# Kernel optimization log

Measured on AMD Instinct MI355X. Metric: run time of the kernel, lower is better.

## Reference

```python
import jax, jax.numpy as jnp
import numpy as np

# Network dims (see init_kwargs)
T, B, N_IN, N_HID, N_OUT = 1000, 256, 128, 512, 128
DT = 0.05
SPIKE_R = 20.0
K_M = 0.2
R_HID = 0.1 + 1.0 / N_HID   # Rs[k] = R + 1/sizes[k]
THRESH = 0.0
V_RESET = 0.0
SIGMA_V = 50.0
I0 = 700.0
ASC_AMP = np.array([-1.0, 1.0], np.float32)
ASC_R = np.array([1.0, -1.0], np.float32)
ASC_K = np.array([3.0, 30.0], np.float32)


def setup_inputs() -> dict:
    key = jax.random.key(0)
    ks = jax.random.split(key, 5)
    s_in = 1.0 / np.sqrt(N_IN)
    s_hid = 1.0 / np.sqrt(N_HID)
    return {
        "inputs": jax.random.normal(ks[0], (T, B, N_IN), jnp.float32),
        "W_in": jax.random.uniform(ks[1], (N_HID, N_IN), jnp.float32, -s_in, s_in),
        "b_in": jnp.zeros((N_HID,), jnp.float32),
        "W_rec": jax.random.uniform(ks[2], (N_HID, N_HID), jnp.float32, -s_hid, s_hid),
        "W_out": jax.random.uniform(ks[3], (N_OUT, N_HID), jnp.float32, -s_hid, s_hid),
        "b_out": jnp.zeros((N_OUT,), jnp.float32),
    }


def reference(inputs, W_in, b_in, W_rec, W_out, b_out):
    """BNN3L forward: per timestep, hidden GLIFR layer receives the average of
    the input projection (current-step placeholder spikes) and the recurrent
    projection of its own spikes delayed by 1 step; the output placeholder
    stores the linear readout of the current hidden spikes.
    Returns stacked output-layer spikes_all: [T, B, N_OUT]."""
    asc_amp = jnp.asarray(ASC_AMP)[:, None, None]
    asc_r = jnp.asarray(ASC_R)[:, None, None]
    asc_k = jnp.asarray(ASC_K)[:, None, None]

    def step(carry, x_t):
        v, asc, s = carry  # v,s: [B,H]; asc: [2,B,H]
        # average of the two incoming connections (n_in = 2)
        y = (x_t @ W_in.T + b_in + s @ W_rec.T) * 0.5
        # after-spike currents (Euler)
        asc = asc * (1.0 - DT * asc_k) + DT * asc_r * asc_amp * s
        i_tot = y + asc.sum(0) + I0
        # membrane voltage with continuous soft reset driven by firing rate s
        v = v * (1.0 - DT * K_M) * (1.0 - DT * s) + DT * s * V_RESET \
            + DT * K_M * R_HID * i_tot
        # rate-coded "spike" output
        s = SPIKE_R * jax.nn.sigmoid((v - THRESH) / SIGMA_V)
        # output placeholder: linear readout of current hidden spikes (delay 1 forced)
        out = s @ W_out.T + b_out
        return (v, asc, s), out

    v0 = jnp.zeros((B, N_HID), jnp.float32)
    asc0 = jnp.zeros((2, B, N_HID), jnp.float32)
    s0 = jnp.zeros((B, N_HID), jnp.float32)
    _, outs = jax.lax.scan(step, (v0, asc0, s0), inputs)
    return outs
```

## Files before the change

kernel.cpp:

```cpp
#include <hip/hip_runtime.h>

#define T_STEPS 1000
#define BATCH   256
#define NIN     128
#define NHID    512
#define NOUT    128
#define ROWS    16
#define HGRP    4
#define HCOLS   128
#define NCLU    16
#define CLUSZ   4

typedef _Float16 half8   __attribute__((ext_vector_type(8)));
typedef float    floatx4 __attribute__((ext_vector_type(4)));

__device__ __forceinline__ half8 f8_to_h8(const float* __restrict__ p) {
  floatx4 lo = *(const floatx4*)p;
  floatx4 hi = *(const floatx4*)(p + 4);
  half8 r;
#pragma unroll
  for (int i = 0; i < 4; ++i) { r[i] = (_Float16)lo[i]; r[i + 4] = (_Float16)hi[i]; }
  return r;
}

#define EX_OFF 1024

__global__ void init_ws_kernel(char* __restrict__ ws) {
  size_t idx = (size_t)blockIdx.x * blockDim.x + threadIdx.x;
  ((int4*)(ws + EX_OFF))[idx] = make_int4(0, 0, 0, 0);
  if (blockIdx.x == 0 && threadIdx.x < NCLU)
    *(unsigned int*)(ws + threadIdx.x * 64) = 0u;
}

#define PBUF 131072

__global__ __launch_bounds__(256, 1) void bnn_cluster_kernel(
    const float* __restrict__ X,
    const float* __restrict__ Win,
    const float* __restrict__ bin,
    const float* __restrict__ Wrec,
    const float* __restrict__ Wout,
    const float* __restrict__ bout,
    float* __restrict__ out,
    char* __restrict__ ws)
{
  __shared__ __attribute__((aligned(16))) char smem[135168];
  const int tid = threadIdx.x;
  const int l   = tid & 63;
  const int w   = tid >> 6;
  const int lr  = l & 15;
  const int lq  = l >> 4;
  const int bi  = blockIdx.x & 15;
  const int hj  = blockIdx.x >> 4;
  const int m0  = bi * ROWS;
  const int cw  = hj * HCOLS + w * 32;
  const int oj  = hj * 32;
  const int tw  = w & 1;
  const int kh  = w >> 1;

  unsigned int* cnt = (unsigned int*)(ws + (size_t)bi * 64);
  _Float16* ex = (_Float16*)(ws + EX_OFF);

#pragma unroll
  for (int tt = 0; tt < 2; ++tt)
#pragma unroll
    for (int kk = 0; kk < 16; ++kk) {
      half8 v = f8_to_h8(Wrec + (size_t)(cw + tt*16 + lr) * NHID + kk*32 + lq*8);
      *(half8*)(smem + (((w*2 + tt)*16 + kk) * 64 + l) * 16) = v;
    }

  half8 win[2][4];
#pragma unroll
  for (int tt = 0; tt < 2; ++tt)
#pragma unroll
    for (int kk = 0; kk < 4; ++kk)
      win[tt][kk] = f8_to_h8(Win + (size_t)(cw + tt*16 + lr) * NIN + kk*32 + lq*8);

  half8 wo[8];
#pragma unroll
  for (int i = 0; i < 8; ++i)
    wo[i] = f8_to_h8(Wout + (size_t)(oj + tw*16 + lr) * NHID + (kh*8 + i)*32 + lq*8);

  const float binv0 = bin[cw + lr];
  const float binv1 = bin[cw + 16 + lr];
  const float bo    = bout[oj + tw*16 + lr];

  float v[8], a0[8], a1[8], sp[8];
#pragma unroll
  for (int i = 0; i < 8; ++i) { v[i] = 0.f; a0[i] = 0.f; a1[i] = 0.f; sp[i] = 0.f; }

  floatx4 rop;
  rop[0] = rop[1] = rop[2] = rop[3] = 0.f;

  const float C_VI = (float)(0.05 * 0.2 * (0.1 + 1.0 / 512.0));

#pragma unroll 1
  for (int t = 0; t <= T_STEPS; ++t) {
    floatx4 xlo[4], xhi[4];
    if (t < T_STEPS) {
      const float* xt = X + ((size_t)t * BATCH + m0 + lr) * NIN + lq * 8;
#pragma unroll
      for (int kk = 0; kk < 4; ++kk) {
        xlo[kk] = *(const floatx4*)(xt + kk * 32);
        xhi[kk] = *(const floatx4*)(xt + kk * 32 + 4);
      }
    }

    __syncthreads();
    if (tid == 0) {
      __threadfence();
      atomicAdd(cnt, 1u);
      const unsigned int tgt = (unsigned int)CLUSZ * (unsigned int)(t + 1);
      while (__hip_atomic_load(cnt, __ATOMIC_RELAXED, __HIP_MEMORY_SCOPE_AGENT) < tgt)
        __builtin_amdgcn_s_sleep(2);
    }
    __syncthreads();
    __threadfence();

    const _Float16* sprev = ex + (size_t)(t & 1) * 131072 + (size_t)bi * 8192;
    half8 sfr[16];
#pragma unroll
    for (int kk = 0; kk < 16; ++kk)
      sfr[kk] = *(const half8*)(sprev + kk * 512 + l * 8);

    if (t >= 2 && w < 2) {
      floatx4 pp = *(const floatx4*)(smem + PBUF + ((t - 1) & 1) * 2048 + tw * 1024 + l * 16);
      float* op = out + ((size_t)(t - 2) * BATCH + m0 + lq * 4) * NOUT + oj + tw * 16 + lr;
#pragma unroll
      for (int r = 0; r < 4; ++r) op[(size_t)r * NOUT] = rop[r] + pp[r] + bo;
    }

    if (t >= 1) {
      floatx4 rp;
      rp[0] = rp[1] = rp[2] = rp[3] = 0.f;
#pragma unroll
      for (int i = 0; i < 8; ++i)
        rp = __builtin_amdgcn_mfma_f32_16x16x32_f16(sfr[kh*8 + i], wo[i], rp, 0, 0, 0);
      if (w >= 2) *(floatx4*)(smem + PBUF + (t & 1) * 2048 + tw * 1024 + l * 16) = rp;
      else        rop = rp;
    }

    if (t < T_STEPS) {
      floatx4 acc[2];
      acc[0][0] = acc[0][1] = acc[0][2] = acc[0][3] = binv0;
      acc[1][0] = acc[1][1] = acc[1][2] = acc[1][3] = binv1;
#pragma unroll
      for (int kk = 0; kk < 16; ++kk) {
#pragma unroll
        for (int tt = 0; tt < 2; ++tt) {
          half8 wb = *(const half8*)(smem + (((w*2 + tt)*16 + kk) * 64 + l) * 16);
          acc[tt] = __builtin_amdgcn_mfma_f32_16x16x32_f16(sfr[kk], wb, acc[tt], 0, 0, 0);
        }
      }
#pragma unroll
      for (int kk = 0; kk < 4; ++kk) {
        half8 xa;
#pragma unroll
        for (int i = 0; i < 4; ++i) {
          xa[i]     = (_Float16)xlo[kk][i];
          xa[i + 4] = (_Float16)xhi[kk][i];
        }
#pragma unroll
        for (int tt = 0; tt < 2; ++tt)
          xa, acc[tt] = __builtin_amdgcn_mfma_f32_16x16x32_f16(xa, win[tt][kk], acc[tt], 0, 0, 0);
      }

      _Float16* scur = ex + (size_t)((t + 1) & 1) * 131072 + (size_t)bi * 8192;
#pragma unroll
      for (int tt = 0; tt < 2; ++tt)
#pragma unroll
        for (int r = 0; r < 4; ++r) {
          const int i = tt*4 + r;
          const float y  = 0.5f * acc[tt][r];
          a0[i] = a0[i] * 0.85f - 0.05f * sp[i];
          a1[i] = a1[i] * -0.5f - 0.05f * sp[i];
          const float it = y + a0[i] + a1[i] + 700.0f;
          v[i] = v[i] * 0.99f * (1.0f - 0.05f * sp[i]) + C_VI * it;
          const float s = 20.0f / (1.0f + __expf(-0.02f * v[i]));
          sp[i] = s;
          const int koff  = tt*16 + lr;
          const int lane2 = (lq*4 + r) + 16*(koff >> 3);
          scur[(hj*4 + w)*512 + lane2*8 + (koff & 7)] = (_Float16)s;
        }
    }
  }

  __syncthreads();
  if (w < 2) {
    floatx4 pp = *(const floatx4*)(smem + PBUF + (T_STEPS & 1) * 2048 + tw * 1024 + l * 16);
    float* op = out + ((size_t)(T_STEPS - 1) * BATCH + m0 + lq * 4) * NOUT + oj + tw * 16 + lr;
#pragma unroll
    for (int r = 0; r < 4; ++r) op[(size_t)r * NOUT] = rop[r] + pp[r] + bo;
  }
}

extern "C" void kernel_launch(void* const* d_in, const int* in_sizes, int n_in,
                              void* d_out, int out_size, void* d_ws, size_t ws_size,
                              hipStream_t stream) {
  const float* X    = (const float*)d_in[0];
  const float* Win  = (const float*)d_in[1];
  const float* bin  = (const float*)d_in[2];
  const float* Wrec = (const float*)d_in[3];
  const float* Wout = (const float*)d_in[4];
  const float* bout = (const float*)d_in[5];
  float* out = (float*)d_out;
  char* ws = (char*)d_ws;

  hipLaunchKernelGGL(init_ws_kernel, dim3(128), dim3(256), 0, stream, ws);
  hipLaunchKernelGGL(bnn_cluster_kernel, dim3(NCLU * HGRP), dim3(256), 0, stream,
                     X, Win, bin, Wrec, Wout, bout, out, ws);
}
```

Baseline: 9.236 ms.

## Replace cluster atomic counter barrier with per-wave flag handshakes

Swaps the per-cluster atomicAdd counter barrier (one thread spinning with sleep, surrounded by __syncthreads and threadfences) for per-wave ready flags. Each wave stages its spike fragment in LDS, publishes it to global memory with relaxed agent-scope stores, then sets its own flag. Consumer waves poll the 16 flags with a ballot, so no thread spins alone and the full fences are gone. This cuts cross-block synchronisation latency on every timestep, but it depends on relaxed ordering plus vmcnt waits being enough for visibility, and it adds a block-wide barrier at the end of each step.

```diff
diff --git a/kernel.cpp b/kernel.cpp
--- a/kernel.cpp
+++ b/kernel.cpp
@@ -6,13 +6,11 @@
 #define NHID    512
 #define NOUT    128
 #define ROWS    16
-#define HGRP    4
-#define HCOLS   128
 #define NCLU    16
-#define CLUSZ   4
 
 typedef _Float16 half8   __attribute__((ext_vector_type(8)));
 typedef float    floatx4 __attribute__((ext_vector_type(4)));
+typedef unsigned long long u64;
 
 __device__ __forceinline__ half8 f8_to_h8(const float* __restrict__ p) {
   floatx4 lo = *(const floatx4*)p;
@@ -23,18 +21,17 @@
   return r;
 }
 
-#define EX_OFF 1024
+#define DATA_OFF 32768
 
 __global__ void init_ws_kernel(char* __restrict__ ws) {
   size_t idx = (size_t)blockIdx.x * blockDim.x + threadIdx.x;
-  ((int4*)(ws + EX_OFF))[idx] = make_int4(0, 0, 0, 0);
-  if (blockIdx.x == 0 && threadIdx.x < NCLU)
-    *(unsigned int*)(ws + threadIdx.x * 64) = 0u;
-}
-
-#define PBUF 131072
-
-__global__ __launch_bounds__(256, 1) void bnn_cluster_kernel(
+  ((int4*)ws)[idx] = make_int4(0, 0, 0, 0);
+}
+
+#define PBUF  131072
+#define STAGE 135168
+
+__global__ __launch_bounds__(256, 1) void bnn_flag_kernel(
     const float* __restrict__ X,
     const float* __restrict__ Win,
     const float* __restrict__ bin,
@@ -44,7 +41,7 @@
     float* __restrict__ out,
     char* __restrict__ ws)
 {
-  __shared__ __attribute__((aligned(16))) char smem[135168];
+  __shared__ __attribute__((aligned(16))) char smem[139264];
   const int tid = threadIdx.x;
   const int l   = tid & 63;
   const int w   = tid >> 6;
@@ -53,13 +50,13 @@
   const int bi  = blockIdx.x & 15;
   const int hj  = blockIdx.x >> 4;
   const int m0  = bi * ROWS;
-  const int cw  = hj * HCOLS + w * 32;
+  const int cw  = hj * 128 + w * 32;
   const int oj  = hj * 32;
   const int tw  = w & 1;
   const int kh  = w >> 1;
-
-  unsigned int* cnt = (unsigned int*)(ws + (size_t)bi * 64);
-  _Float16* ex = (_Float16*)(ws + EX_OFF);
+  const int myf = hj * 4 + w;
+
+  unsigned* flags = (unsigned*)ws;
 
 #pragma unroll
   for (int tt = 0; tt < 2; ++tt)
@@ -93,6 +90,8 @@
   rop[0] = rop[1] = rop[2] = rop[3] = 0.f;
 
   const float C_VI = (float)(0.05 * 0.2 * (0.1 + 1.0 / 512.0));
+
+  __syncthreads();
 
 #pragma unroll 1
   for (int t = 0; t <= T_STEPS; ++t) {
@@ -106,22 +105,28 @@
       }
     }
 
-    __syncthreads();
-    if (tid == 0) {
-      __threadfence();
-      atomicAdd(cnt, 1u);
-      const unsigned int tgt = (unsigned int)CLUSZ * (unsigned int)(t + 1);
-      while (__hip_atomic_load(cnt, __ATOMIC_RELAXED, __HIP_MEMORY_SCOPE_AGENT) < tgt)
-        __builtin_amdgcn_s_sleep(2);
-    }
-    __syncthreads();
-    __threadfence();
-
-    const _Float16* sprev = ex + (size_t)(t & 1) * 131072 + (size_t)bi * 8192;
+    if (t > 0) {
+      const unsigned* flg = flags + (size_t)((t & 1) * 16 + bi) * 256;
+      u64 rdy;
+      do {
+        unsigned fv = 0xFFFFFFFFu;
+        if (l < 16)
+          fv = __hip_atomic_load(flg + l * 16, __ATOMIC_RELAXED, __HIP_MEMORY_SCOPE_AGENT);
+        rdy = __ballot(fv >= (unsigned)t);
+      } while (rdy != 0xFFFFFFFFFFFFFFFFull);
+    }
+    __builtin_amdgcn_sched_barrier(0);
+
+    const u64* dq = (const u64*)(ws + DATA_OFF + (size_t)(t & 1) * 262144
+                                 + (size_t)bi * 16384);
     half8 sfr[16];
 #pragma unroll
-    for (int kk = 0; kk < 16; ++kk)
-      sfr[kk] = *(const half8*)(sprev + kk * 512 + l * 8);
+    for (int kk = 0; kk < 16; ++kk) {
+      union { u64 u[2]; half8 h; } cv;
+      cv.u[0] = __hip_atomic_load(dq + kk*128 + l*2,     __ATOMIC_RELAXED, __HIP_MEMORY_SCOPE_AGENT);
+      cv.u[1] = __hip_atomic_load(dq + kk*128 + l*2 + 1, __ATOMIC_RELAXED, __HIP_MEMORY_SCOPE_AGENT);
+      sfr[kk] = cv.h;
+    }
 
     if (t >= 2 && w < 2) {
       floatx4 pp = *(const floatx4*)(smem + PBUF + ((t - 1) & 1) * 2048 + tw * 1024 + l * 16);
@@ -162,10 +167,9 @@
         }
 #pragma unroll
         for (int tt = 0; tt < 2; ++tt)
-          xa, acc[tt] = __builtin_amdgcn_mfma_f32_16x16x32_f16(xa, win[tt][kk], acc[tt], 0, 0, 0);
-      }
-
-      _Float16* scur = ex + (size_t)((t + 1) & 1) * 131072 + (size_t)bi * 8192;
+          acc[tt] = __builtin_amdgcn_mfma_f32_16x16x32_f16(xa, win[tt][kk], acc[tt], 0, 0, 0);
+      }
+
 #pragma unroll
       for (int tt = 0; tt < 2; ++tt)
 #pragma unroll
@@ -180,12 +184,28 @@
           sp[i] = s;
           const int koff  = tt*16 + lr;
           const int lane2 = (lq*4 + r) + 16*(koff >> 3);
-          scur[(hj*4 + w)*512 + lane2*8 + (koff & 7)] = (_Float16)s;
+          *(_Float16*)(smem + STAGE + w*1024 + lane2*16 + (koff & 7)*2) = (_Float16)s;
         }
-    }
+
+      asm volatile("s_waitcnt lgkmcnt(0)" ::: "memory");
+      __builtin_amdgcn_sched_barrier(0);
+      u64 s0 = *(const u64*)(smem + STAGE + w*1024 + l*16);
+      u64 s1 = *(const u64*)(smem + STAGE + w*1024 + l*16 + 8);
+      u64* dst = (u64*)(ws + DATA_OFF + (size_t)((t + 1) & 1) * 262144
+                        + (size_t)bi * 16384) + (size_t)myf * 128 + l * 2;
+      __hip_atomic_store(dst,     s0, __ATOMIC_RELAXED, __HIP_MEMORY_SCOPE_AGENT);
+      __hip_atomic_store(dst + 1, s1, __ATOMIC_RELAXED, __HIP_MEMORY_SCOPE_AGENT);
+      asm volatile("s_waitcnt vmcnt(0)" ::: "memory");
+      __builtin_amdgcn_sched_barrier(0);
+      if (l == 0) {
+        unsigned* fl = flags + (size_t)(((t + 1) & 1) * 16 + bi) * 256 + (size_t)myf * 16;
+        __hip_atomic_store(fl, (unsigned)(t + 1), __ATOMIC_RELAXED, __HIP_MEMORY_SCOPE_AGENT);
+      }
+    }
+
+    __syncthreads();
   }
 
-  __syncthreads();
   if (w < 2) {
     floatx4 pp = *(const floatx4*)(smem + PBUF + (T_STEPS & 1) * 2048 + tw * 1024 + l * 16);
     float* op = out + ((size_t)(T_STEPS - 1) * BATCH + m0 + lq * 4) * NOUT + oj + tw * 16 + lr;
@@ -206,7 +226,7 @@
   float* out = (float*)d_out;
   char* ws = (char*)d_ws;
 
-  hipLaunchKernelGGL(init_ws_kernel, dim3(128), dim3(256), 0, stream, ws);
-  hipLaunchKernelGGL(bnn_cluster_kernel, dim3(NCLU * HGRP), dim3(256), 0, stream,
+  hipLaunchKernelGGL(init_ws_kernel, dim3(136), dim3(256), 0, stream, ws);
+  hipLaunchKernelGGL(bnn_flag_kernel, dim3(64), dim3(256), 0, stream,
                      X, Win, bin, Wrec, Wout, bout, out, ws);
 }
```

Result: faster. 8.339 ms (-9.7%).
